# Performance work log

Measured on AMD Instinct MI355X. Metric: run time of the kernel, lower is better.

Reference implementation:

```python
import jax, jax.numpy as jnp
import numpy as np

D_MODEL = 1024
NUM_HEADS = 16
HEAD_DIM = D_MODEL // NUM_HEADS


def setup_inputs() -> dict:
    key = jax.random.key(0)
    ks = jax.random.split(key, 9)
    s = D_MODEL ** -0.5  # roughly like nn.Linear init scale
    x = jax.random.normal(ks[0], (4, 2048, D_MODEL), dtype=jnp.float32)
    Wq = jax.random.normal(ks[1], (D_MODEL, D_MODEL), dtype=jnp.float32) * s
    bq = jax.random.normal(ks[2], (D_MODEL,), dtype=jnp.float32) * s
    Wk = jax.random.normal(ks[3], (D_MODEL, D_MODEL), dtype=jnp.float32) * s
    bk = jax.random.normal(ks[4], (D_MODEL,), dtype=jnp.float32) * s
    Wv = jax.random.normal(ks[5], (D_MODEL, D_MODEL), dtype=jnp.float32) * s
    bv = jax.random.normal(ks[6], (D_MODEL,), dtype=jnp.float32) * s
    Wo = jax.random.normal(ks[7], (D_MODEL, D_MODEL), dtype=jnp.float32) * s
    bo = jax.random.normal(ks[8], (D_MODEL,), dtype=jnp.float32) * s
    return {"x": x, "Wq": Wq, "bq": bq, "Wk": Wk, "bk": bk,
            "Wv": Wv, "bv": bv, "Wo": Wo, "bo": bo}


def reference(x, Wq, bq, Wk, bk, Wv, bv, Wo, bo):
    B, S, D = x.shape
    H, Dh = NUM_HEADS, HEAD_DIM
    scale = Dh ** -0.5
    # nn.Linear: x @ W.T + b
    q = (x @ Wq.T + bq).reshape(B, S, H, Dh)
    k = (x @ Wk.T + bk).reshape(B, S, H, Dh)
    v = (x @ Wv.T + bv).reshape(B, S, H, Dh)
    # scores: (B, H, S, S), full materialization as in the original bmm path
    dp = scale * jnp.einsum('bqhd,bkhd->bhqk', q, k)
    att = jax.nn.softmax(dp, axis=-1)
    out = jnp.einsum('bhqk,bkhd->bqhd', att, v).reshape(B, S, D)
    return out @ Wo.T + bo
```

## Files before the change

### kernel.cpp

```cpp
#include <hip/hip_runtime.h>
#include <stdint.h>

typedef __attribute__((ext_vector_type(8))) __bf16 bf16x8;
typedef __attribute__((ext_vector_type(4))) float floatx4;

#define DEV __device__ __forceinline__

DEV unsigned short f2bf(float f) {
    union { float f; unsigned u; } uf; uf.f = f;
    unsigned u = uf.u;
    unsigned r = (u + 0x7fffu + ((u >> 16) & 1u)) >> 16;
    return (unsigned short)r;
}

DEV float fast_exp2(float x) {
#if __has_builtin(__builtin_amdgcn_exp2f)
    return __builtin_amdgcn_exp2f(x);
#else
    return exp2f(x);
#endif
}

DEV unsigned pack_trunc2(float lo, float hi) {
    return __builtin_amdgcn_perm(__float_as_uint(hi), __float_as_uint(lo), 0x07060302u);
}

DEV void async16(const void* g, void* l) {
    __builtin_amdgcn_global_load_lds(
        (const __attribute__((address_space(1))) void*)g,
        (__attribute__((address_space(3))) void*)l, 16, 0, 0);
}

__global__ void cast_bf16_kernel(const float* __restrict__ src,
                                 unsigned short* __restrict__ dst, int n4) {
    int i = blockIdx.x * blockDim.x + threadIdx.x;
    if (i >= n4) return;
    float4 v = reinterpret_cast<const float4*>(src)[i];
    ushort4 o;
    o.x = f2bf(v.x); o.y = f2bf(v.y); o.z = f2bf(v.z); o.w = f2bf(v.w);
    reinterpret_cast<ushort4*>(dst)[i] = o;
}

template <int MODE>
__global__ __launch_bounds__(256)
void gemm128(const unsigned short* __restrict__ A,
             const unsigned short* __restrict__ B,
             const float* __restrict__ bias,
             unsigned short* __restrict__ q_ws,
             unsigned short* __restrict__ k_ws,
             unsigned short* __restrict__ v_ws,
             float* __restrict__ fout) {
    constexpr int K = 1024;
    __shared__ alignas(16) unsigned short smem[128 * 136];
    unsigned short* sA = smem;
    unsigned short* sB = smem + 128 * 64;
    unsigned short* sT = smem;

    const int tid = threadIdx.x;
    const int w = tid >> 6, lane = tid & 63, quad = lane >> 4, l16 = lane & 15;
    const int wr = w >> 1, wc = w & 1;
    const int bm = blockIdx.y, bn = blockIdx.x;
    const int arow0 = bm * 128, brow0 = bn * 128;

    floatx4 acc[4][4];
#pragma unroll
    for (int i = 0; i < 4; i++)
#pragma unroll
        for (int j = 0; j < 4; j++) acc[i][j] = (floatx4){0.f, 0.f, 0.f, 0.f};

    for (int k0 = 0; k0 < K; k0 += 64) {
#pragma unroll
        for (int i = 0; i < 4; i++) {
            int cb = i * 256 + w * 64;
            int ci = cb + lane;
            int row = ci >> 3, cl = ci & 7, cs = cl ^ (row & 7);
            async16(A + (size_t)(arow0 + row) * K + k0 + cs * 8, (char*)sA + cb * 16);
            async16(B + (size_t)(brow0 + row) * K + k0 + cs * 8, (char*)sB + cb * 16);
        }
        __syncthreads();
#pragma unroll
        for (int kk = 0; kk < 2; kk++) {
            bf16x8 aF[4], bF[4];
#pragma unroll
            for (int i = 0; i < 4; i++) {
                int row = wr * 64 + i * 16 + l16;
                int c = kk * 4 + quad, ph = c ^ (row & 7);
                aF[i] = *reinterpret_cast<const bf16x8*>(sA + row * 64 + ph * 8);
            }
#pragma unroll
            for (int j = 0; j < 4; j++) {
                int row = wc * 64 + j * 16 + l16;
                int c = kk * 4 + quad, ph = c ^ (row & 7);
                bF[j] = *reinterpret_cast<const bf16x8*>(sB + row * 64 + ph * 8);
            }
#pragma unroll
            for (int i = 0; i < 4; i++)
#pragma unroll
                for (int j = 0; j < 4; j++)
                    acc[i][j] = __builtin_amdgcn_mfma_f32_16x16x32_bf16(
                        aF[i], bF[j], acc[i][j], 0, 0, 0);
        }
        __syncthreads();
    }

    if (MODE == 1) {
#pragma unroll
        for (int j = 0; j < 4; j++) {
            const int gcol = brow0 + wc * 64 + j * 16 + l16;
            const float bia = bias[gcol];
#pragma unroll
            for (int i = 0; i < 4; i++) {
#pragma unroll
                for (int r = 0; r < 4; r++) {
                    int grow = arow0 + wr * 64 + i * 16 + quad * 4 + r;
                    fout[(size_t)grow * 1024 + gcol] = acc[i][j][r] + bia;
                }
            }
        }
    } else if (bn < 16) {
        unsigned short* dst = (bn < 8) ? q_ws : k_ws;
        const float sc = (bn < 8) ? 0.18033688f : 1.0f;
#pragma unroll
        for (int j = 0; j < 4; j++) {
            const int gcol = brow0 + wc * 64 + j * 16 + l16;
            const int nn = gcol & 1023, h = nn >> 6, d = nn & 63;
            const float bia = bias[gcol];
#pragma unroll
            for (int i = 0; i < 4; i++) {
                int s_base = arow0 + wr * 64 + i * 16 + quad * 4;
                int bb = s_base >> 11, s4 = s_base & 2047;
                int bh = bb * 16 + h;
#pragma unroll
                for (int r = 0; r < 4; r++) {
                    dst[((size_t)bh * 2048 + (s4 + r)) * 64 + d] =
                        f2bf((acc[i][j][r] + bia) * sc);
                }
            }
        }
    } else {
#pragma unroll
        for (int j = 0; j < 4; j++) {
            const int c = wc * 64 + j * 16 + l16;
            const float bia = bias[brow0 + c];
#pragma unroll
            for (int i = 0; i < 4; i++) {
                int v_hi = wr * 4 + i;
#pragma unroll
                for (int r = 0; r < 4; r++) {
                    int v = (quad * 4 + r) * 8 + v_hi;
                    sT[c * 136 + v] = f2bf(acc[i][j][r] + bia);
                }
            }
        }
        __syncthreads();
        const int bb = bm >> 4, blk = bm & 15;
        const int chunk = tid & 15;
#pragma unroll
        for (int it = 0; it < 8; it++) {
            int row = (tid >> 4) + it * 16;
            int h = (bn - 16) * 2 + (row >> 6), d = row & 63;
            ushort4 lo = *reinterpret_cast<const ushort4*>(sT + row * 136 + chunk * 8);
            ushort4 hi = *reinterpret_cast<const ushort4*>(sT + row * 136 + chunk * 8 + 4);
            size_t off = ((size_t)(bb * 16 + h) * 64 + d) * 2048 + blk * 128 + chunk * 8;
            *reinterpret_cast<ushort4*>(v_ws + off) = lo;
            *reinterpret_cast<ushort4*>(v_ws + off + 4) = hi;
        }
    }
}

__global__ __launch_bounds__(256)
void attn_kernel(const unsigned short* __restrict__ q_ws,
                 const unsigned short* __restrict__ k_ws,
                 const unsigned short* __restrict__ v_ws,
                 unsigned short* __restrict__ o_ws) {
    constexpr int PP = 152;
    __shared__ alignas(16) unsigned short sK[128 * 64];
    __shared__ alignas(16) unsigned short sVt[64 * 128];
    __shared__ alignas(16) unsigned short sP[4][16 * PP];

    const int tid = threadIdx.x;
    const int w = tid >> 6, lane = tid & 63, quad = lane >> 4, l16 = lane & 15;
    const int id = blockIdx.x;
    const int bh = (id >> 8) * 8 + (id & 7);
    const int q0 = ((id >> 3) & 31) * 64;
    const size_t base = (size_t)bh * 2048 * 64;

    bf16x8 aQ[2];
    {
        int qrow = q0 + w * 16 + l16;
        const unsigned short* qp = q_ws + base + (size_t)qrow * 64 + quad * 8;
        aQ[0] = *reinterpret_cast<const bf16x8*>(qp);
        aQ[1] = *reinterpret_cast<const bf16x8*>(qp + 32);
    }

    const __bf16 one = (__bf16)1.0f;
    const bf16x8 vOnes = {one, one, one, one, one, one, one, one};

    floatx4 oAcc[4], rsAcc;
#pragma unroll
    for (int j = 0; j < 4; j++) oAcc[j] = (floatx4){0.f, 0.f, 0.f, 0.f};
    rsAcc = (floatx4){0.f, 0.f, 0.f, 0.f};

    for (int t = 0; t < 16; t++) {
        const int kv0 = t * 128;
#pragma unroll
        for (int i = 0; i < 4; i++) {
            int cb = i * 256 + w * 64;
            int ci = cb + lane;
            {
                int row = ci >> 3, cl = ci & 7, cs = cl ^ (row & 7);
                async16(k_ws + base + (size_t)(kv0 + row) * 64 + cs * 8,
                        (char*)sK + cb * 16);
            }
            {
                int row = ci >> 4, cl = ci & 15, cs = cl ^ (row & 15);
                async16(v_ws + base + (size_t)row * 2048 + kv0 + cs * 8,
                        (char*)sVt + cb * 16);
            }
        }
        __syncthreads();

        floatx4 sAcc[8];
#pragma unroll
        for (int j = 0; j < 8; j++) sAcc[j] = (floatx4){0.f, 0.f, 0.f, 0.f};
#pragma unroll
        for (int kk = 0; kk < 2; kk++) {
#pragma unroll
            for (int j = 0; j < 8; j++) {
                int krow = j * 16 + l16;
                int c = kk * 4 + quad, ph = c ^ (krow & 7);
                bf16x8 bK = *reinterpret_cast<const bf16x8*>(sK + krow * 64 + ph * 8);
                sAcc[j] = __builtin_amdgcn_mfma_f32_16x16x32_bf16(aQ[kk], bK, sAcc[j], 0, 0, 0);
            }
        }

#pragma unroll
        for (int r = 0; r < 4; r++) {
            float e[8];
#pragma unroll
            for (int j = 0; j < 8; j++) e[j] = fast_exp2(sAcc[j][r]);
            uint4 pk;
            pk.x = pack_trunc2(e[0], e[1]);
            pk.y = pack_trunc2(e[2], e[3]);
            pk.z = pack_trunc2(e[4], e[5]);
            pk.w = pack_trunc2(e[6], e[7]);
            *reinterpret_cast<uint4*>(&sP[w][(quad * 4 + r) * PP + l16 * 8]) = pk;
        }
        asm volatile("s_waitcnt lgkmcnt(0)" ::: "memory");

        bf16x8 aP[4];
#pragma unroll
        for (int ks = 0; ks < 4; ks++)
            aP[ks] = *reinterpret_cast<const bf16x8*>(&sP[w][l16 * PP + ks * 32 + quad * 8]);
#pragma unroll
        for (int jd = 0; jd < 4; jd++) {
            int drow = jd * 16 + l16;
#pragma unroll
            for (int ks = 0; ks < 4; ks++) {
                int c = ks * 4 + quad, ph = c ^ (drow & 15);
                bf16x8 bV = *reinterpret_cast<const bf16x8*>(sVt + drow * 128 + ph * 8);
                oAcc[jd] = __builtin_amdgcn_mfma_f32_16x16x32_bf16(aP[ks], bV, oAcc[jd], 0, 0, 0);
            }
        }
#pragma unroll
        for (int ks = 0; ks < 4; ks++)
            rsAcc = __builtin_amdgcn_mfma_f32_16x16x32_bf16(aP[ks], vOnes, rsAcc, 0, 0, 0);
        __syncthreads();
    }

    float inv[4];
#pragma unroll
    for (int r = 0; r < 4; r++) inv[r] = 1.0f / rsAcc[r];
    const int bb = bh >> 4, h = bh & 15;
#pragma unroll
    for (int jd = 0; jd < 4; jd++) {
        int d = jd * 16 + l16;
#pragma unroll
        for (int r = 0; r < 4; r++) {
            int s = q0 + w * 16 + quad * 4 + r;
            float v = oAcc[jd][r] * inv[r];
            o_ws[((size_t)bb * 2048 + s) * 1024 + h * 64 + d] = f2bf(v);
        }
    }
}

extern "C" void kernel_launch(void* const* d_in, const int* in_sizes, int n_in,
                              void* d_out, int out_size, void* d_ws, size_t ws_size,
                              hipStream_t stream) {
    const float* x  = (const float*)d_in[0];
    const float* Wq = (const float*)d_in[1];
    const float* bq = (const float*)d_in[2];
    const float* Wk = (const float*)d_in[3];
    const float* bk = (const float*)d_in[4];
    const float* Wv = (const float*)d_in[5];
    const float* bv = (const float*)d_in[6];
    const float* Wo = (const float*)d_in[7];
    const float* bo = (const float*)d_in[8];
    float* out = (float*)d_out;

    char* ws = (char*)d_ws;
    unsigned short* xb   = (unsigned short*)(ws);
    unsigned short* wqkv = (unsigned short*)(ws + (16ull << 20));
    unsigned short* wo   = (unsigned short*)(ws + (22ull << 20));
    float*          bqkv = (float*)(ws + (24ull << 20));
    unsigned short* q_ws = (unsigned short*)(ws + (25ull << 20));
    unsigned short* k_ws = (unsigned short*)(ws + (41ull << 20));
    unsigned short* v_ws = (unsigned short*)(ws + (57ull << 20));
    unsigned short* o_ws = xb;

    const int n4x = 8192 * 1024 / 4;
    cast_bf16_kernel<<<n4x / 256, 256, 0, stream>>>(x, xb, n4x);
    const int n4w = 1024 * 1024 / 4;
    cast_bf16_kernel<<<n4w / 256, 256, 0, stream>>>(Wq, wqkv, n4w);
    cast_bf16_kernel<<<n4w / 256, 256, 0, stream>>>(Wk, wqkv + 1024 * 1024, n4w);
    cast_bf16_kernel<<<n4w / 256, 256, 0, stream>>>(Wv, wqkv + 2 * 1024 * 1024, n4w);
    cast_bf16_kernel<<<n4w / 256, 256, 0, stream>>>(Wo, wo, n4w);
    hipMemcpyAsync(bqkv,        bq, 4096, hipMemcpyDeviceToDevice, stream);
    hipMemcpyAsync(bqkv + 1024, bk, 4096, hipMemcpyDeviceToDevice, stream);
    hipMemcpyAsync(bqkv + 2048, bv, 4096, hipMemcpyDeviceToDevice, stream);

    gemm128<0><<<dim3(24, 64), 256, 0, stream>>>(xb, wqkv, bqkv, q_ws, k_ws, v_ws, nullptr);
    attn_kernel<<<2048, 256, 0, stream>>>(q_ws, k_ws, v_ws, o_ws);
    gemm128<1><<<dim3(8, 64), 256, 0, stream>>>(o_ws, wo, bo, nullptr, nullptr, nullptr, out);
}
```

Measured before the change: 304.3 us.

## Stage GEMM epilogues through LDS, merge weight casts, hoist attention load addresses

```diff
diff --git a/kernel.cpp b/kernel.cpp
--- a/kernel.cpp
+++ b/kernel.cpp
@@ -39,6 +39,34 @@
     ushort4 o;
     o.x = f2bf(v.x); o.y = f2bf(v.y); o.z = f2bf(v.z); o.w = f2bf(v.w);
     reinterpret_cast<ushort4*>(dst)[i] = o;
+}
+
+__global__ void cast_w_kernel(const float* __restrict__ Wq, const float* __restrict__ Wk,
+                              const float* __restrict__ Wv, const float* __restrict__ Wo,
+                              const float* __restrict__ bq, const float* __restrict__ bk,
+                              const float* __restrict__ bv,
+                              unsigned short* __restrict__ wqkv,
+                              unsigned short* __restrict__ wo,
+                              float* __restrict__ bqkv) {
+    const int NW = 262144;
+    int i = blockIdx.x * blockDim.x + threadIdx.x;
+    if (i < 4 * NW) {
+        int seg = i >> 18, off = i & (NW - 1);
+        const float* src = (seg == 0) ? Wq : (seg == 1) ? Wk : (seg == 2) ? Wv : Wo;
+        unsigned short* dst = (seg < 3) ? (wqkv + seg * 1048576) : wo;
+        float4 v = reinterpret_cast<const float4*>(src)[off];
+        ushort4 o;
+        o.x = f2bf(v.x); o.y = f2bf(v.y); o.z = f2bf(v.z); o.w = f2bf(v.w);
+        reinterpret_cast<ushort4*>(dst)[off] = o;
+    } else {
+        int j = i - 4 * NW;
+        if (j < 768) {
+            int seg = j >> 8, off = j & 255;
+            const float* src = (seg == 0) ? bq : (seg == 1) ? bk : bv;
+            reinterpret_cast<float4*>(bqkv)[j] =
+                reinterpret_cast<const float4*>(src)[off];
+        }
+    }
 }
 
 template <int MODE>
@@ -55,6 +83,7 @@
     unsigned short* sA = smem;
     unsigned short* sB = smem + 128 * 64;
     unsigned short* sT = smem;
+    float* sT32 = reinterpret_cast<float*>(smem);
 
     const int tid = threadIdx.x;
     const int w = tid >> 6, lane = tid & 63, quad = lane >> 4, l16 = lane & 15;
@@ -105,16 +134,30 @@
 
     if (MODE == 1) {
 #pragma unroll
-        for (int j = 0; j < 4; j++) {
-            const int gcol = brow0 + wc * 64 + j * 16 + l16;
-            const float bia = bias[gcol];
-#pragma unroll
-            for (int i = 0; i < 4; i++) {
-#pragma unroll
-                for (int r = 0; r < 4; r++) {
-                    int grow = arow0 + wr * 64 + i * 16 + quad * 4 + r;
-                    fout[(size_t)grow * 1024 + gcol] = acc[i][j][r] + bia;
+        for (int ch = 0; ch < 2; ch++) {
+            if (ch) __syncthreads();
+            if (wr == ch) {
+#pragma unroll
+                for (int j = 0; j < 4; j++) {
+                    const int c = wc * 64 + j * 16 + l16;
+                    const float bia = bias[brow0 + c];
+#pragma unroll
+                    for (int i = 0; i < 4; i++) {
+                        int s_loc = i * 16 + quad * 4;
+#pragma unroll
+                        for (int r = 0; r < 4; r++)
+                            sT32[(s_loc + r) * 132 + c] = acc[i][j][r] + bia;
+                    }
                 }
+            }
+            __syncthreads();
+            const int cpos = (tid & 31) * 4;
+#pragma unroll
+            for (int it = 0; it < 8; it++) {
+                int s_loc = (tid >> 5) + it * 8;
+                int grow = arow0 + ch * 64 + s_loc;
+                float4 vv = *reinterpret_cast<const float4*>(sT32 + s_loc * 132 + cpos);
+                *reinterpret_cast<float4*>(fout + (size_t)grow * 1024 + brow0 + cpos) = vv;
             }
         }
     } else if (bn < 16) {
@@ -122,20 +165,28 @@
         const float sc = (bn < 8) ? 0.18033688f : 1.0f;
 #pragma unroll
         for (int j = 0; j < 4; j++) {
-            const int gcol = brow0 + wc * 64 + j * 16 + l16;
-            const int nn = gcol & 1023, h = nn >> 6, d = nn & 63;
-            const float bia = bias[gcol];
+            const int c = wc * 64 + j * 16 + l16;
+            const float bia = bias[brow0 + c];
 #pragma unroll
             for (int i = 0; i < 4; i++) {
-                int s_base = arow0 + wr * 64 + i * 16 + quad * 4;
-                int bb = s_base >> 11, s4 = s_base & 2047;
-                int bh = bb * 16 + h;
-#pragma unroll
-                for (int r = 0; r < 4; r++) {
-                    dst[((size_t)bh * 2048 + (s4 + r)) * 64 + d] =
-                        f2bf((acc[i][j][r] + bia) * sc);
-                }
-            }
+                int s_loc = wr * 64 + i * 16 + quad * 4;
+#pragma unroll
+                for (int r = 0; r < 4; r++)
+                    sT[(s_loc + r) * 136 + c] = f2bf((acc[i][j][r] + bia) * sc);
+            }
+        }
+        __syncthreads();
+        const int nnbase = (bn & 7) * 128;
+        const int c0 = (tid & 15) * 8;
+        const int h = (nnbase + c0) >> 6, d = c0 & 63;
+#pragma unroll
+        for (int it = 0; it < 8; it++) {
+            int s_loc = (tid >> 4) + it * 16;
+            int s = arow0 + s_loc;
+            int bb = s >> 11, s4 = s & 2047;
+            uint4 vdat = *reinterpret_cast<const uint4*>(sT + s_loc * 136 + c0);
+            *reinterpret_cast<uint4*>(
+                dst + ((size_t)(bb * 16 + h) * 2048 + s4) * 64 + d) = vdat;
         }
     } else {
 #pragma unroll
@@ -193,6 +244,26 @@
         aQ[1] = *reinterpret_cast<const bf16x8*>(qp + 32);
     }
 
+    const unsigned short* kptr[4];
+    const unsigned short* vptr[4];
+    char* klds[4];
+    char* vlds[4];
+#pragma unroll
+    for (int i = 0; i < 4; i++) {
+        int cb = i * 256 + w * 64;
+        int ci = cb + lane;
+        {
+            int row = ci >> 3, cl = ci & 7, cs = cl ^ (row & 7);
+            kptr[i] = k_ws + base + (size_t)row * 64 + cs * 8;
+            klds[i] = (char*)sK + cb * 16;
+        }
+        {
+            int row = ci >> 4, cl = ci & 15, cs = cl ^ (row & 15);
+            vptr[i] = v_ws + base + (size_t)row * 2048 + cs * 8;
+            vlds[i] = (char*)sVt + cb * 16;
+        }
+    }
+
     const __bf16 one = (__bf16)1.0f;
     const bf16x8 vOnes = {one, one, one, one, one, one, one, one};
 
@@ -205,18 +276,8 @@
         const int kv0 = t * 128;
 #pragma unroll
         for (int i = 0; i < 4; i++) {
-            int cb = i * 256 + w * 64;
-            int ci = cb + lane;
-            {
-                int row = ci >> 3, cl = ci & 7, cs = cl ^ (row & 7);
-                async16(k_ws + base + (size_t)(kv0 + row) * 64 + cs * 8,
-                        (char*)sK + cb * 16);
-            }
-            {
-                int row = ci >> 4, cl = ci & 15, cs = cl ^ (row & 15);
-                async16(v_ws + base + (size_t)row * 2048 + kv0 + cs * 8,
-                        (char*)sVt + cb * 16);
-            }
+            async16(kptr[i] + (size_t)kv0 * 64, klds[i]);
+            async16(vptr[i] + kv0, vlds[i]);
         }
         __syncthreads();
 
@@ -310,14 +371,8 @@
 
     const int n4x = 8192 * 1024 / 4;
     cast_bf16_kernel<<<n4x / 256, 256, 0, stream>>>(x, xb, n4x);
-    const int n4w = 1024 * 1024 / 4;
-    cast_bf16_kernel<<<n4w / 256, 256, 0, stream>>>(Wq, wqkv, n4w);
-    cast_bf16_kernel<<<n4w / 256, 256, 0, stream>>>(Wk, wqkv + 1024 * 1024, n4w);
-    cast_bf16_kernel<<<n4w / 256, 256, 0, stream>>>(Wv, wqkv + 2 * 1024 * 1024, n4w);
-    cast_bf16_kernel<<<n4w / 256, 256, 0, stream>>>(Wo, wo, n4w);
-    hipMemcpyAsync(bqkv,        bq, 4096, hipMemcpyDeviceToDevice, stream);
-    hipMemcpyAsync(bqkv + 1024, bk, 4096, hipMemcpyDeviceToDevice, stream);
-    hipMemcpyAsync(bqkv + 2048, bv, 4096, hipMemcpyDeviceToDevice, stream);
+    cast_w_kernel<<<4099, 256, 0, stream>>>(Wq, Wk, Wv, Wo, bq, bk, bv,
+                                            wqkv, wo, bqkv);
 
     gemm128<0><<<dim3(24, 64), 256, 0, stream>>>(xb, wqkv, bqkv, q_ws, k_ws, v_ws, nullptr);
     attn_kernel<<<2048, 256, 0, stream>>>(q_ws, k_ws, v_ws, o_ws);
```

New measurement: 298.5 us. No clear change (-1.9%).
